# Kernel tuning notes

Hardware: AMD Instinct MI355X
Metric: run time of the kernel (lower is better)

Reference implementation:

```python
import jax, jax.numpy as jnp
import numpy as np

N_NODES = 50000
N_EDGES = 800000
D_IN = 64
D_OUT = 64


def setup_inputs() -> dict:
    key = jax.random.key(0)
    k1, k2, k3, k4 = jax.random.split(key, 4)
    x = jax.random.normal(k1, (N_NODES, D_IN), dtype=jnp.float32)
    edge_index = jax.random.randint(k2, (2, N_EDGES), 0, N_NODES, dtype=jnp.int64)
    W = jax.random.normal(k3, (D_IN, D_OUT), dtype=jnp.float32) * (1.0 / np.sqrt(D_IN))
    b = jax.random.normal(k4, (D_OUT,), dtype=jnp.float32) * 0.01
    return {"x": x, "edge_index": edge_index, "W": W, "b": b}


def reference(x, edge_index, W, b):
    N = x.shape[0]
    # Add self-loops (PyG GCNConv default add_self_loops=True)
    loop = jnp.arange(N, dtype=edge_index.dtype)
    src = jnp.concatenate([edge_index[0], loop])  # source j
    dst = jnp.concatenate([edge_index[1], loop])  # target i
    # Linear transform first (standard GCNConv: theta then propagate)
    xw = x @ W  # [N, D_OUT]
    # Symmetric degree normalization: deg over targets of (A + I)
    ones = jnp.ones(src.shape[0], dtype=x.dtype)
    deg = jax.ops.segment_sum(ones, dst, num_segments=N)
    dis = jnp.where(deg > 0, jax.lax.rsqrt(jnp.maximum(deg, 1.0)), 0.0)
    norm = dis[src] * dis[dst]  # [E+N]
    # Gather, weight, scatter-add
    msgs = norm[:, None] * xw[src]  # [E+N, D_OUT]
    out = jax.ops.segment_sum(msgs, dst, num_segments=N) + b
    return jax.nn.relu(out)
```

## Files before the change

### kernel.cpp

```cpp
#include <hip/hip_runtime.h>

#define N_NODES 50000
#define N_EDGES 800000
#define D 64
#define FINE_SHIFT 6
#define FINE_NODES 64
#define NBUCK ((N_NODES + FINE_NODES - 1) / FINE_NODES)
#define CAP 1280
#define EPB 8192
#define NPART ((N_EDGES + EPB - 1) / EPB)
#define GRPT (CAP / 256)

typedef _Float16 f16;
typedef __attribute__((ext_vector_type(2))) _Float16 f16x2;
typedef __attribute__((ext_vector_type(4))) _Float16 f16x4;
typedef __attribute__((ext_vector_type(8))) _Float16 f16x8;
typedef __attribute__((ext_vector_type(4))) float f32x4;

__global__ __launch_bounds__(1024) void partition_edges(
    const int* __restrict__ src, const int* __restrict__ dst,
    int* __restrict__ cursor, unsigned int* __restrict__ binned)
{
    __shared__ int hist[NBUCK];
    __shared__ int start_s[NBUCK];
    __shared__ int lcur[NBUCK];
    __shared__ int base_s[NBUCK];
    __shared__ unsigned int staged[EPB];

    int tid = threadIdx.x;
    int eb  = blockIdx.x * EPB;
    int total = N_EDGES - eb; if (total > EPB) total = EPB;

    for (int i = tid; i < NBUCK; i += 1024) hist[i] = 0;
    __syncthreads();

    unsigned int rec[8];
    #pragma unroll
    for (int u = 0; u < 8; ++u) {
        int j = u * 1024 + tid;
        if (j < total) {
            unsigned int t = (unsigned int)dst[eb + j];
            rec[u] = (t << 16) | (unsigned int)src[eb + j];
            atomicAdd(&hist[t >> FINE_SHIFT], 1);
        } else rec[u] = 0xFFFFFFFFu;
    }
    __syncthreads();

    if (tid < 64) {
        int b0 = tid * 13;
        int v[13]; int run = 0;
        #pragma unroll
        for (int j = 0; j < 13; ++j) {
            int idx = b0 + j;
            int c = (idx < NBUCK) ? hist[idx] : 0;
            v[j] = run; run += c;
        }
        int s = run;
        #pragma unroll
        for (int off = 1; off < 64; off <<= 1) {
            int t = __shfl_up(s, off);
            if (tid >= off) s += t;
        }
        int excl = s - run;
        #pragma unroll
        for (int j = 0; j < 13; ++j) {
            int idx = b0 + j;
            if (idx < NBUCK) { start_s[idx] = excl + v[j]; lcur[idx] = excl + v[j]; }
        }
    }
    __syncthreads();

    for (int i = tid; i < NBUCK; i += 1024) {
        int c = hist[i];
        base_s[i] = c ? atomicAdd(&cursor[i], c) : 0;
    }
    #pragma unroll
    for (int u = 0; u < 8; ++u) {
        unsigned int v = rec[u];
        if (v != 0xFFFFFFFFu) {
            int cb = v >> (16 + FINE_SHIFT);
            int p  = atomicAdd(&lcur[cb], 1);
            staged[p] = v;
        }
    }
    __syncthreads();

    for (int i = tid; i < total; i += 1024) {
        unsigned int v = staged[i];
        int cb = v >> (16 + FINE_SHIFT);
        int gp = base_s[cb] + (i - start_s[cb]);
        if (gp < CAP) binned[(size_t)cb * CAP + gp] = v;
    }
}

__global__ __launch_bounds__(256) void xws_fused(
    const int* __restrict__ cursor, const unsigned int* __restrict__ binned,
    const float* __restrict__ x, const float* __restrict__ W,
    f16* __restrict__ xwsh)
{
    __shared__ f16 xsH[64][72];
    __shared__ f16 WtH[64][72];
    __shared__ float dis_l[64];
    __shared__ int h[64];

    int bu = blockIdx.x, tid = threadIdx.x;
    int nb = bu * FINE_NODES;

    if (tid < 64) h[tid] = 0;
    __syncthreads();
    int cnt = cursor[bu]; if (cnt > CAP) cnt = CAP;
    const unsigned int* br = binned + (size_t)bu * CAP;
    for (int i = tid; i < cnt; i += 256)
        atomicAdd(&h[(br[i] >> 16) & 63], 1);

    const float4* x4 = (const float4*)x;
    for (int j = tid; j < 1024; j += 256) {
        int row = j >> 4, c4 = (j & 15) * 4;
        float4 v;
        if (nb + row < N_NODES) v = x4[(size_t)(nb + row) * 16 + (j & 15)];
        else { v.x = v.y = v.z = v.w = 0.f; }
        f16x4 hv = { (f16)v.x, (f16)v.y, (f16)v.z, (f16)v.w };
        *(f16x4*)&xsH[row][c4] = hv;
    }
    for (int j = tid; j < 4096; j += 256) {
        int k = j >> 6, n = j & 63;
        WtH[n][k] = (f16)W[j];
    }
    __syncthreads();
    if (tid < 64) dis_l[tid] = rsqrtf((float)h[tid] + 1.0f);
    __syncthreads();

    int wave = tid >> 6, lane = tid & 63;
    int m = lane & 15, q = lane >> 4;

    f16x8 a0 = *(const f16x8*)&xsH[wave * 16 + m][q * 8];
    f16x8 a1 = *(const f16x8*)&xsH[wave * 16 + m][32 + q * 8];

    f32x4 acc[4];
    #pragma unroll
    for (int t = 0; t < 4; ++t) {
        int n0 = t * 16;
        f16x8 b0 = *(const f16x8*)&WtH[n0 + m][q * 8];
        f16x8 b1 = *(const f16x8*)&WtH[n0 + m][32 + q * 8];
        f32x4 z = { 0.f, 0.f, 0.f, 0.f };
        z = __builtin_amdgcn_mfma_f32_16x16x32_f16(a0, b0, z, 0, 0, 0);
        acc[t] = __builtin_amdgcn_mfma_f32_16x16x32_f16(a1, b1, z, 0, 0, 0);
    }

    #pragma unroll
    for (int t = 0; t < 4; ++t) {
        int n0 = t * 16;
        #pragma unroll
        for (int r = 0; r < 4; ++r) {
            int row = q * 4 + r;
            xsH[wave * 16 + row][n0 + m] = (f16)(acc[t][r] * dis_l[wave * 16 + row]);
        }
    }
    __syncthreads();

    for (int j = tid; j < 512; j += 256) {
        int row = j >> 3, seg = (j & 7) * 8;
        if (nb + row < N_NODES)
            *(f16x8*)&xwsh[(size_t)(nb + row) * D + seg] = *(const f16x8*)&xsH[row][seg];
    }
}

__global__ __launch_bounds__(256) void gather_out(
    const int* __restrict__ cursor, const unsigned int* __restrict__ binned,
    const f16* __restrict__ xwsh, const float* __restrict__ b,
    float* __restrict__ out)
{
    __shared__ unsigned short ssrc[CAP];
    __shared__ int h[64], off_s[64], cur[64];

    int cb = blockIdx.x, tid = threadIdx.x;
    int wave = tid >> 6, lane = tid & 63;
    int nb = cb * FINE_NODES;
    int cnt = cursor[cb]; if (cnt > CAP) cnt = CAP;
    const unsigned int* br = binned + (size_t)cb * CAP;

    if (tid < 64) h[tid] = 0;
    __syncthreads();

    unsigned int rec[GRPT];
    #pragma unroll
    for (int u = 0; u < GRPT; ++u) {
        int j = u * 256 + tid;
        if (j < cnt) {
            rec[u] = br[j];
            atomicAdd(&h[(rec[u] >> 16) & 63], 1);
        } else rec[u] = 0xFFFFFFFFu;
    }
    __syncthreads();

    if (tid < 64) {
        int v = h[tid], s = v;
        #pragma unroll
        for (int off = 1; off < 64; off <<= 1) {
            int t = __shfl_up(s, off);
            if (tid >= off) s += t;
        }
        off_s[tid] = s - v;
        cur[tid]   = s - v;
    }
    __syncthreads();

    #pragma unroll
    for (int u = 0; u < GRPT; ++u) {
        unsigned int v = rec[u];
        if (v != 0xFFFFFFFFu) {
            int p = atomicAdd(&cur[(v >> 16) & 63], 1);
            ssrc[p] = (unsigned short)(v & 0xFFFFu);
        }
    }
    __syncthreads();

    const f16x2* xw2 = (const f16x2*)xwsh;
    float2* out2 = (float2*)out;
    int c32 = lane & 31;
    int hid = lane >> 5;
    float2 bl2 = ((const float2*)b)[c32];

    for (int i = 0; i < 16; ++i) {
        int nl = wave * 16 + i;
        int n  = nb + nl;
        if (n >= N_NODES) break;
        int off = off_s[nl], c = h[nl];
        float dn = rsqrtf((float)c + 1.0f);

        float2 acc; acc.x = 0.f; acc.y = 0.f;
        if (hid == 0) {
            f16x2 sv = xw2[(size_t)n * 32 + c32];
            acc.x = (float)sv.x; acc.y = (float)sv.y;
        }
        int k = off + hid, e = off + c;
        for (; k + 6 < e; k += 8) {
            int s0 = ssrc[k], s1 = ssrc[k + 2], s2 = ssrc[k + 4], s3 = ssrc[k + 6];
            f16x2 v0 = xw2[(size_t)s0 * 32 + c32];
            f16x2 v1 = xw2[(size_t)s1 * 32 + c32];
            f16x2 v2 = xw2[(size_t)s2 * 32 + c32];
            f16x2 v3 = xw2[(size_t)s3 * 32 + c32];
            acc.x += ((float)v0.x + (float)v1.x) + ((float)v2.x + (float)v3.x);
            acc.y += ((float)v0.y + (float)v1.y) + ((float)v2.y + (float)v3.y);
        }
        for (; k < e; k += 2) {
            f16x2 v = xw2[(size_t)ssrc[k] * 32 + c32];
            acc.x += (float)v.x; acc.y += (float)v.y;
        }
        acc.x += __shfl(acc.x, lane + 32);
        acc.y += __shfl(acc.y, lane + 32);
        if (hid == 0) {
            float2 r;
            r.x = fmaxf(bl2.x + dn * acc.x, 0.f);
            r.y = fmaxf(bl2.y + dn * acc.y, 0.f);
            out2[(size_t)n * 32 + c32] = r;
        }
    }
}

extern "C" void kernel_launch(void* const* d_in, const int* in_sizes, int n_in,
                              void* d_out, int out_size, void* d_ws, size_t ws_size,
                              hipStream_t stream) {
    const float* x  = (const float*)d_in[0];
    const int*   ei = (const int*)d_in[1];
    const float* W  = (const float*)d_in[2];
    const float* b  = (const float*)d_in[3];

    const int* src = ei;
    const int* dst = ei + N_EDGES;
    float* out = (float*)d_out;

    f16*          xwsh   = (f16*)d_ws;
    int*          cursor = (int*)(xwsh + (size_t)N_NODES * D);
    unsigned int* binned = (unsigned int*)(cursor + 784);

    hipMemsetAsync(cursor, 0, 784 * sizeof(int), stream);
    partition_edges<<<NPART, 1024, 0, stream>>>(src, dst, cursor, binned);
    xws_fused<<<NBUCK, 256, 0, stream>>>(cursor, binned, x, W, xwsh);
    gather_out<<<NBUCK, 256, 0, stream>>>(cursor, binned, xwsh, b, out);
}
```

Baseline: 120.8 us.

## Pretranspose W once to fp16, load x straight into MFMA registers, halve partition tile

Block 0 of the partition kernel now writes a transposed fp16 copy of W to workspace once, so each of the 782 xws blocks does a vectorized copy instead of a strided fp32 transpose into shared memory. The x tile is loaded directly from global into the MFMA A-operand registers, skipping the shared-memory staging and one barrier. Degree rsqrt is computed per lane in registers. Separately, edges per partition block drop from 8192 to 4096, doubling the partition grid for more parallelism at the cost of more global cursor atomics.

```diff
diff --git a/kernel.cpp b/kernel.cpp
--- a/kernel.cpp
+++ b/kernel.cpp
@@ -7,19 +7,19 @@
 #define FINE_NODES 64
 #define NBUCK ((N_NODES + FINE_NODES - 1) / FINE_NODES)
 #define CAP 1280
-#define EPB 8192
+#define EPB 4096
 #define NPART ((N_EDGES + EPB - 1) / EPB)
 #define GRPT (CAP / 256)
 
 typedef _Float16 f16;
 typedef __attribute__((ext_vector_type(2))) _Float16 f16x2;
-typedef __attribute__((ext_vector_type(4))) _Float16 f16x4;
 typedef __attribute__((ext_vector_type(8))) _Float16 f16x8;
 typedef __attribute__((ext_vector_type(4))) float f32x4;
 
 __global__ __launch_bounds__(1024) void partition_edges(
     const int* __restrict__ src, const int* __restrict__ dst,
-    int* __restrict__ cursor, unsigned int* __restrict__ binned)
+    int* __restrict__ cursor, unsigned int* __restrict__ binned,
+    const float* __restrict__ W, f16* __restrict__ Wt16)
 {
     __shared__ int hist[NBUCK];
     __shared__ int start_s[NBUCK];
@@ -31,12 +31,19 @@
     int eb  = blockIdx.x * EPB;
     int total = N_EDGES - eb; if (total > EPB) total = EPB;
 
+    if (blockIdx.x == 0) {
+        for (int j = tid; j < 4096; j += 1024) {
+            int n = j >> 6, k = j & 63;
+            Wt16[j] = (f16)W[k * 64 + n];
+        }
+    }
+
     for (int i = tid; i < NBUCK; i += 1024) hist[i] = 0;
     __syncthreads();
 
-    unsigned int rec[8];
-    #pragma unroll
-    for (int u = 0; u < 8; ++u) {
+    unsigned int rec[4];
+    #pragma unroll
+    for (int u = 0; u < 4; ++u) {
         int j = u * 1024 + tid;
         if (j < total) {
             unsigned int t = (unsigned int)dst[eb + j];
@@ -75,7 +82,7 @@
         base_s[i] = c ? atomicAdd(&cursor[i], c) : 0;
     }
     #pragma unroll
-    for (int u = 0; u < 8; ++u) {
+    for (int u = 0; u < 4; ++u) {
         unsigned int v = rec[u];
         if (v != 0xFFFFFFFFu) {
             int cb = v >> (16 + FINE_SHIFT);
@@ -95,12 +102,11 @@
 
 __global__ __launch_bounds__(256) void xws_fused(
     const int* __restrict__ cursor, const unsigned int* __restrict__ binned,
-    const float* __restrict__ x, const float* __restrict__ W,
+    const float* __restrict__ x, const f16* __restrict__ Wt16,
     f16* __restrict__ xwsh)
 {
-    __shared__ f16 xsH[64][72];
     __shared__ f16 WtH[64][72];
-    __shared__ float dis_l[64];
+    __shared__ f16 park[64][72];
     __shared__ int h[64];
 
     int bu = blockIdx.x, tid = threadIdx.x;
@@ -108,33 +114,33 @@
 
     if (tid < 64) h[tid] = 0;
     __syncthreads();
+
     int cnt = cursor[bu]; if (cnt > CAP) cnt = CAP;
     const unsigned int* br = binned + (size_t)bu * CAP;
     for (int i = tid; i < cnt; i += 256)
         atomicAdd(&h[(br[i] >> 16) & 63], 1);
 
-    const float4* x4 = (const float4*)x;
-    for (int j = tid; j < 1024; j += 256) {
-        int row = j >> 4, c4 = (j & 15) * 4;
-        float4 v;
-        if (nb + row < N_NODES) v = x4[(size_t)(nb + row) * 16 + (j & 15)];
-        else { v.x = v.y = v.z = v.w = 0.f; }
-        f16x4 hv = { (f16)v.x, (f16)v.y, (f16)v.z, (f16)v.w };
-        *(f16x4*)&xsH[row][c4] = hv;
-    }
-    for (int j = tid; j < 4096; j += 256) {
-        int k = j >> 6, n = j & 63;
-        WtH[n][k] = (f16)W[j];
-    }
-    __syncthreads();
-    if (tid < 64) dis_l[tid] = rsqrtf((float)h[tid] + 1.0f);
+    for (int j = tid; j < 512; j += 256) {
+        int row = j >> 3, seg = (j & 7) * 8;
+        *(f16x8*)&WtH[row][seg] = *(const f16x8*)&Wt16[row * 64 + seg];
+    }
     __syncthreads();
 
     int wave = tid >> 6, lane = tid & 63;
     int m = lane & 15, q = lane >> 4;
 
-    f16x8 a0 = *(const f16x8*)&xsH[wave * 16 + m][q * 8];
-    f16x8 a1 = *(const f16x8*)&xsH[wave * 16 + m][32 + q * 8];
+    int ar = nb + wave * 16 + m;
+    if (ar >= N_NODES) ar = N_NODES - 1;
+    const float4* x4 = (const float4*)x;
+    size_t rb = (size_t)ar * 16;
+    float4 p0 = x4[rb + q * 2];
+    float4 p1 = x4[rb + q * 2 + 1];
+    float4 p2 = x4[rb + 8 + q * 2];
+    float4 p3 = x4[rb + 8 + q * 2 + 1];
+    f16x8 a0 = { (f16)p0.x, (f16)p0.y, (f16)p0.z, (f16)p0.w,
+                 (f16)p1.x, (f16)p1.y, (f16)p1.z, (f16)p1.w };
+    f16x8 a1 = { (f16)p2.x, (f16)p2.y, (f16)p2.z, (f16)p2.w,
+                 (f16)p3.x, (f16)p3.y, (f16)p3.z, (f16)p3.w };
 
     f32x4 acc[4];
     #pragma unroll
@@ -147,21 +153,23 @@
         acc[t] = __builtin_amdgcn_mfma_f32_16x16x32_f16(a1, b1, z, 0, 0, 0);
     }
 
+    float disr[4];
+    #pragma unroll
+    for (int r = 0; r < 4; ++r)
+        disr[r] = rsqrtf((float)h[wave * 16 + q * 4 + r] + 1.0f);
     #pragma unroll
     for (int t = 0; t < 4; ++t) {
         int n0 = t * 16;
         #pragma unroll
-        for (int r = 0; r < 4; ++r) {
-            int row = q * 4 + r;
-            xsH[wave * 16 + row][n0 + m] = (f16)(acc[t][r] * dis_l[wave * 16 + row]);
-        }
+        for (int r = 0; r < 4; ++r)
+            park[wave * 16 + q * 4 + r][n0 + m] = (f16)(acc[t][r] * disr[r]);
     }
     __syncthreads();
 
     for (int j = tid; j < 512; j += 256) {
         int row = j >> 3, seg = (j & 7) * 8;
         if (nb + row < N_NODES)
-            *(f16x8*)&xwsh[(size_t)(nb + row) * D + seg] = *(const f16x8*)&xsH[row][seg];
+            *(f16x8*)&xwsh[(size_t)(nb + row) * D + seg] = *(const f16x8*)&park[row][seg];
     }
 }
 
@@ -273,9 +281,10 @@
     f16*          xwsh   = (f16*)d_ws;
     int*          cursor = (int*)(xwsh + (size_t)N_NODES * D);
     unsigned int* binned = (unsigned int*)(cursor + 784);
+    f16*          Wt16   = (f16*)(binned + (size_t)NBUCK * CAP);
 
     hipMemsetAsync(cursor, 0, 784 * sizeof(int), stream);
-    partition_edges<<<NPART, 1024, 0, stream>>>(src, dst, cursor, binned);
-    xws_fused<<<NBUCK, 256, 0, stream>>>(cursor, binned, x, W, xwsh);
+    partition_edges<<<NPART, 1024, 0, stream>>>(src, dst, cursor, binned, W, Wt16);
+    xws_fused<<<NBUCK, 256, 0, stream>>>(cursor, binned, x, Wt16, xwsh);
     gather_out<<<NBUCK, 256, 0, stream>>>(cursor, binned, xwsh, b, out);
 }
```

Result: no change. 120.5 us (-0.3%).
